# Optimization experiments

Hardware: AMD Instinct MI355X
Metric: run time of the kernel (lower is better)

## Reference

```python
import jax, jax.numpy as jnp
import numpy as np
from jax import lax

H = 1024      # hidden_size
E = 512       # embedding_size
K = 4         # max_num_children
NCLASS = 10000
EOS = NCLASS
N = 256       # number of tree nodes (complete K-ary tree, topo order)
L = 512       # number of annotation vectors


def setup_inputs() -> dict:
    key = jax.random.key(0)
    ks = jax.random.split(key, 16)
    s = 0.05
    rootH = jax.random.normal(ks[0], (1, H), jnp.float32)
    rootC = jax.random.normal(ks[1], (1, H), jnp.float32)
    annotations = jax.random.normal(ks[2], (L, H), jnp.float32)
    values = jax.random.randint(ks[3], (N,), 0, NCLASS, jnp.int32)
    idx = np.arange(N)
    parent = jnp.asarray(np.maximum(idx - 1, 0) // K, jnp.int32)
    slot = jnp.asarray(np.maximum(idx - 1, 0) % K, jnp.int32)
    # learned parameters
    emb = jax.random.normal(ks[4], (NCLASS + 1, E), jnp.float32) * s
    W_ih = jax.random.normal(ks[5], (K, 4 * H, E + H), jnp.float32) * s
    W_hh = jax.random.normal(ks[6], (K, 4 * H, H), jnp.float32) * s
    b_ih = jax.random.normal(ks[7], (K, 4 * H), jnp.float32) * s
    b_hh = jax.random.normal(ks[8], (K, 4 * H), jnp.float32) * s
    W_att = jax.random.normal(ks[9], (H, H), jnp.float32) * s
    b_att = jax.random.normal(ks[10], (H,), jnp.float32) * s
    W_pre = jax.random.normal(ks[11], (H, 2 * H), jnp.float32) * s
    b_pre = jax.random.normal(ks[12], (H,), jnp.float32) * s
    W_out = jax.random.normal(ks[13], (NCLASS + 1, H), jnp.float32) * s
    b_out = jax.random.normal(ks[14], (NCLASS + 1,), jnp.float32) * s
    return dict(rootH=rootH, rootC=rootC, annotations=annotations, values=values,
                parent=parent, slot=slot, emb=emb, W_ih=W_ih, W_hh=W_hh,
                b_ih=b_ih, b_hh=b_hh, W_att=W_att, b_att=b_att,
                W_pre=W_pre, b_pre=b_pre, W_out=W_out, b_out=b_out)


def reference(rootH, rootC, annotations, values, parent, slot, emb,
              W_ih, W_hh, b_ih, b_hh, W_att, b_att, W_pre, b_pre, W_out, b_out):
    # attention_hidden(annotations), computed once (align_type=1)
    ahv = annotations @ W_att.T + b_att            # [L, H]
    rootH0, rootC0 = rootH[0], rootC[0]            # [H]

    def step(carry, xs):
        Hbuf, Cbuf, etbuf, loss = carry
        i, v, p, k = xs
        # child LSTMCell update from parent state (slot k picks the cell)
        x = jnp.concatenate([emb[values[p]], etbuf[p]])            # [E+H]
        gates = W_ih[k] @ x + b_ih[k] + W_hh[k] @ Hbuf[p] + b_hh[k]  # [4H]
        ig, fg, gg, og = jnp.split(gates, 4)
        c_child = jax.nn.sigmoid(fg) * Cbuf[p] + jax.nn.sigmoid(ig) * jnp.tanh(gg)
        h_child = jax.nn.sigmoid(og) * jnp.tanh(c_child)
        is_root = i == 0
        h = jnp.where(is_root, rootH0, h_child)
        c = jnp.where(is_root, rootC0, c_child)
        # attention over annotations (softmax over L)
        att_logits = ahv @ h                                        # [L]
        probs = jax.nn.softmax(att_logits)
        ctx = probs @ annotations                                   # [H]
        et = jnp.tanh(W_pre @ jnp.concatenate([h, ctx]) + b_pre)    # [H]
        # output: softmax then CrossEntropyLoss (faithful double softmax)
        out_logits = W_out @ et + b_out                             # [NCLASS+1]
        p_out = jax.nn.softmax(out_logits)
        ls = jax.nn.log_softmax(p_out)
        nl = -ls[v]
        nl = jnp.where(v == EOS, nl / 5.0, nl)
        Hbuf = Hbuf.at[i].set(h)
        Cbuf = Cbuf.at[i].set(c)
        etbuf = etbuf.at[i].set(et)
        return (Hbuf, Cbuf, etbuf, loss + nl), None

    z = jnp.zeros((N, H), jnp.float32)
    init = (z, z, z, jnp.float32(0.0))
    xs = (jnp.arange(N, dtype=jnp.int32), values, parent, slot)
    (Hb, Cb, eb, loss), _ = lax.scan(step, init, xs)
    return loss
```

## Files before the change

kernel.cpp:

```cpp
#include <hip/hip_runtime.h>
#include <hip/hip_bf16.h>
#include <math.h>

#define HD 1024
#define NCLS 10001

typedef short s16x8 __attribute__((ext_vector_type(8)));
typedef unsigned short u16x8 __attribute__((ext_vector_type(8)));
typedef float f32x4 __attribute__((ext_vector_type(4)));
#define MFMA16(a_, b_, c_) __builtin_amdgcn_mfma_f32_16x16x32_bf16((a_), (b_), (c_), 0, 0, 0)

__device__ __forceinline__ float sigf(float x){ return 1.f/(1.f+__expf(-x)); }
__device__ __forceinline__ float tanhfast(float x){
  x = fminf(fmaxf(x,-10.f),10.f);
  float e2 = __expf(2.f*x);
  return (e2-1.f)/(e2+1.f);
}
__device__ __forceinline__ unsigned short f2bf(float f){
  unsigned int u = __float_as_uint(f);
  u += 0x7FFF + ((u >> 16) & 1);
  return (unsigned short)(u >> 16);
}
__device__ __forceinline__ u16x8 pack8(float4 a, float4 b){
  u16x8 r;
  r[0]=f2bf(a.x); r[1]=f2bf(a.y); r[2]=f2bf(a.z); r[3]=f2bf(a.w);
  r[4]=f2bf(b.x); r[5]=f2bf(b.y); r[6]=f2bf(b.z); r[7]=f2bf(b.w);
  return r;
}

__global__ __launch_bounds__(256) void k_cvt8(const float* __restrict__ A, unsigned short* __restrict__ B, int n){
  int i = (blockIdx.x*256 + threadIdx.x)*8;
  if (i < n){
    float4 a = *(const float4*)(A+i);
    float4 b = *(const float4*)(A+i+4);
    *(u16x8*)(B+i) = pack8(a,b);
  }
}

__global__ __launch_bounds__(256) void k_cvtw8(const float* __restrict__ Wih, const float* __restrict__ Whh,
                                               unsigned short* __restrict__ Wb){
  unsigned e8 = (blockIdx.x*256 + threadIdx.x)*8;
  unsigned sr = e8 / 2560;
  unsigned c  = e8 - sr*2560;
  const float* src = (c < 1536) ? (Wih + (size_t)sr*1536 + c) : (Whh + (size_t)sr*1024 + (c-1536));
  float4 a = *(const float4*)src;
  float4 b = *(const float4*)(src+4);
  *(u16x8*)(Wb + e8) = pack8(a,b);
}

__global__ __launch_bounds__(256) void k_cvtpre8(const float* __restrict__ Wpre,
                                                 unsigned short* __restrict__ Bpre, unsigned short* __restrict__ Wc){
  unsigned idx8 = (blockIdx.x*256 + threadIdx.x)*8;
  unsigned row = idx8 >> 11, c = idx8 & 2047;
  float4 a = *(const float4*)(Wpre + idx8);
  float4 b = *(const float4*)(Wpre + idx8 + 4);
  unsigned short* d = (c < 1024) ? (Bpre + (size_t)row*1536 + c) : (Wc + (size_t)row*1024 + (c-1024));
  *(u16x8*)d = pack8(a,b);
}

__global__ __launch_bounds__(256) void k_root(const float* __restrict__ rH, const float* __restrict__ rC,
                                              float* __restrict__ Hb, float* __restrict__ Cb,
                                              unsigned short* __restrict__ XH){
  int t = blockIdx.x*256 + threadIdx.x;
  if (t < HD){ Hb[t]=rH[t]; Cb[t]=rC[t]; XH[t]=f2bf(rH[t]); }
}

__global__ __launch_bounds__(256) void k_xasm(const float* __restrict__ emb, const int* __restrict__ values,
                                              const unsigned short* __restrict__ Etb, const unsigned short* __restrict__ XH,
                                              unsigned short* __restrict__ X, int s, int e){
  int i = s + blockIdx.x;
  if (i >= e) return;
  int slot = (i - s) & 3, j = (i - s) >> 2;
  int p = (i - 1) >> 2;
  unsigned short* xr = X + ((size_t)slot*48 + j) * 2560;
  int tid = threadIdx.x;
  const float* er = emb + (size_t)values[p] * 512;
  if (tid < 64) {
    int c = tid*8;
    float4 a = *(const float4*)(er+c);
    float4 b = *(const float4*)(er+c+4);
    *(u16x8*)(xr+c) = pack8(a,b);
  }
  const unsigned short* et = Etb + (size_t)p * 1024;
  for (int c = tid*4; c < 1024*4; c += 256*4) {}
  for (int c = tid; c < 256; c += 256) {
    ((u16x8*)(xr+512))[c]  = ((const u16x8*)et)[c];
  }
  const unsigned short* hp = XH + (size_t)p * 1536;
  for (int c = tid; c < 128; c += 256) {
    ((u16x8*)(xr+1536))[c] = ((const u16x8*)hp)[c];
  }
  if (tid >= 128 && tid < 256) {
    int c = tid - 128;
    ((u16x8*)(xr+1536))[c+0] = ((const u16x8*)hp)[c+0];
  }
}

template<int MT>
__global__ __launch_bounds__(256) void k_gemm_fb(
    const unsigned short* __restrict__ A, int astride,
    const unsigned short* __restrict__ B, int K,
    const float* __restrict__ bias,
    float* __restrict__ Cf, unsigned short* __restrict__ Cb16,
    int ostride, int coff, int N, int M)
{
  const int mb0 = blockIdx.y * (MT*16);
  const int wv = threadIdx.x >> 6, lane = threadIdx.x & 63;
  const int col = (blockIdx.x*4 + wv)*16 + (lane & 15);
  const int colc = min(col, N-1);
  const int khalf = (lane >> 4) * 8;

  f32x4 acc[MT];
  #pragma unroll
  for (int m = 0; m < MT; ++m) acc[m] = (f32x4){0.f,0.f,0.f,0.f};
  int arow[MT];
  #pragma unroll
  for (int m = 0; m < MT; ++m) arow[m] = min(mb0 + m*16 + (lane & 15), M-1);

  #pragma unroll 4
  for (int kk = 0; kk < K; kk += 32) {
    int kb = kk + khalf;
    s16x8 bfv = *(const s16x8*)(B + (size_t)colc*K + kb);
    #pragma unroll
    for (int m = 0; m < MT; ++m) {
      s16x8 af = *(const s16x8*)(A + (size_t)arow[m]*astride + kb);
      acc[m] = MFMA16(af, bfv, acc[m]);
    }
  }

  const int r0 = (lane >> 4) * 4;
  #pragma unroll
  for (int m = 0; m < MT; ++m) {
    #pragma unroll
    for (int q = 0; q < 4; ++q) {
      int row = mb0 + m*16 + r0 + q;
      if (row < M && col < N) {
        float v = acc[m][q] + (bias ? bias[col] : 0.f);
        size_t off = (size_t)row*ostride + col + coff;
        if (Cb16) Cb16[off] = f2bf(v); else Cf[off] = v;
      }
    }
  }
}

template<int MT, int KITER>
__global__ __launch_bounds__(256) void k_gemm_skzb(
    const unsigned short* __restrict__ A,
    const unsigned short* __restrict__ B, int K,
    float* __restrict__ P, int N, int Mbase, int Mpad,
    int aZ, int bZ, int KS)
{
  const int z = blockIdx.z;
  const int M = (Mbase - z + 3) >> 2;
  const unsigned short* Az = A + (size_t)z*aZ;
  const unsigned short* Bz = B + (size_t)z*bZ;
  const int ks = blockIdx.y;
  const int k0 = ks * (KITER*32);
  const int wv = threadIdx.x >> 6, lane = threadIdx.x & 63;
  const int col = (blockIdx.x*4 + wv)*16 + (lane & 15);
  const int colc = min(col, N-1);
  const int khalf = (lane >> 4) * 8;

  f32x4 acc[MT];
  #pragma unroll
  for (int m = 0; m < MT; ++m) acc[m] = (f32x4){0.f,0.f,0.f,0.f};
  int arow[MT];
  #pragma unroll
  for (int m = 0; m < MT; ++m) arow[m] = min(m*16 + (lane & 15), M-1);

  #pragma unroll 4
  for (int kk = 0; kk < KITER*32; kk += 32) {
    int kb = k0 + kk + khalf;
    s16x8 bfv = *(const s16x8*)(Bz + (size_t)colc*K + kb);
    #pragma unroll
    for (int m = 0; m < MT; ++m) {
      s16x8 af = *(const s16x8*)(Az + (size_t)arow[m]*K + kb);
      acc[m] = MFMA16(af, bfv, acc[m]);
    }
  }

  const int r0 = (lane >> 4) * 4;
  #pragma unroll
  for (int m = 0; m < MT; ++m) {
    #pragma unroll
    for (int q = 0; q < 4; ++q) {
      int row = m*16 + r0 + q;
      if (row < M && col < N)
        P[(((size_t)z*KS + ks)*Mpad + row)*N + col] = acc[m][q];
    }
  }
}

template<int MT>
__global__ __launch_bounds__(256) void k_gemm_skb(
    const unsigned short* __restrict__ A, int astride,
    const unsigned short* __restrict__ B, int K,
    float* __restrict__ P, int N, int M)
{
  const int ks = blockIdx.y;
  const int k0 = ks * 128;
  const int wv = threadIdx.x >> 6, lane = threadIdx.x & 63;
  const int col = (blockIdx.x*4 + wv)*16 + (lane & 15);
  const int colc = min(col, N-1);
  const int khalf = (lane >> 4) * 8;

  f32x4 acc[MT];
  #pragma unroll
  for (int m = 0; m < MT; ++m) acc[m] = (f32x4){0.f,0.f,0.f,0.f};
  int arow[MT];
  #pragma unroll
  for (int m = 0; m < MT; ++m) arow[m] = min(m*16 + (lane & 15), M-1);

  #pragma unroll
  for (int kk = 0; kk < 128; kk += 32) {
    int kb = k0 + kk + khalf;
    s16x8 bfv = *(const s16x8*)(B + (size_t)colc*K + kb);
    #pragma unroll
    for (int m = 0; m < MT; ++m) {
      s16x8 af = *(const s16x8*)(A + (size_t)arow[m]*astride + kb);
      acc[m] = MFMA16(af, bfv, acc[m]);
    }
  }

  const int r0 = (lane >> 4) * 4;
  #pragma unroll
  for (int m = 0; m < MT; ++m) {
    #pragma unroll
    for (int q = 0; q < 4; ++q) {
      int row = m*16 + r0 + q;
      if (row < M && col < N)
        P[((size_t)ks*M + row)*N + col] = acc[m][q];
    }
  }
}

__global__ __launch_bounds__(256) void k_red(const float* __restrict__ P, int KS, int M, int N,
                                             const float* __restrict__ bias, int tanh_flag,
                                             float* __restrict__ Cf, unsigned short* __restrict__ Cb16,
                                             int ostride)
{
  int idx = blockIdx.x*256 + threadIdx.x;
  if (idx >= M*N) return;
  int row = idx / N, col = idx - row*N;
  float s = bias ? bias[col] : 0.f;
  for (int ks = 0; ks < KS; ++ks) s += P[((size_t)ks*M + row)*N + col];
  if (tanh_flag) s = tanhfast(s);
  if (Cb16) Cb16[(size_t)row*ostride + col] = f2bf(s);
  else      Cf  [(size_t)row*ostride + col] = s;
}

__global__ __launch_bounds__(256) void k_soft(const float* __restrict__ P, int KS, int M,
                                              unsigned short* __restrict__ dst)
{
  __shared__ float sm[512];
  __shared__ float red[8];
  const int m = blockIdx.x;
  const int tid = threadIdx.x, wv = tid>>6, ln = tid&63;
  for (int l = tid; l < 512; l += 256) {
    float s = 0.f;
    for (int ks = 0; ks < KS; ++ks) s += P[((size_t)ks*M + m)*512 + l];
    sm[l] = s;
  }
  __syncthreads();
  float mx = -1e30f;
  for (int l=tid; l<512; l+=256) mx = fmaxf(mx, sm[l]);
  #pragma unroll
  for (int o=32;o;o>>=1) mx = fmaxf(mx, __shfl_xor(mx,o,64));
  if (ln==0) red[wv]=mx;
  __syncthreads();
  mx = fmaxf(fmaxf(red[0],red[1]),fmaxf(red[2],red[3]));
  float se = 0.f;
  for (int l=tid; l<512; l+=256){ float ev=__expf(sm[l]-mx); sm[l]=ev; se+=ev; }
  __syncthreads();
  #pragma unroll
  for (int o=32;o;o>>=1) se += __shfl_xor(se,o,64);
  if (ln==0) red[wv]=se;
  __syncthreads();
  float invS = 1.f/(red[0]+red[1]+red[2]+red[3]);
  for (int l=tid; l<512; l+=256) dst[(size_t)m*1536 + l] = f2bf(sm[l]*invS);
}

__global__ __launch_bounds__(256) void k_epi(const float* __restrict__ P,
                                             const float* __restrict__ b_ih, const float* __restrict__ b_hh,
                                             float* __restrict__ Hb, float* __restrict__ Cb,
                                             unsigned short* __restrict__ XH, int s, int e){
  int i = s + blockIdx.x;
  if (i >= e) return;
  int slot = (i - s) & 3, j = (i - s) >> 2;
  int p = (i - 1) >> 2;
  const float* bi = b_ih + (size_t)slot*4096;
  const float* bh = b_hh + (size_t)slot*4096;
  for (int u = threadIdx.x; u < 1024; u += 256) {
    float ig = bi[u]      + bh[u];
    float fg = bi[1024+u] + bh[1024+u];
    float gg = bi[2048+u] + bh[2048+u];
    float og = bi[3072+u] + bh[3072+u];
    #pragma unroll
    for (int ks = 0; ks < 5; ++ks) {
      const float* g = P + (((size_t)slot*5 + ks)*48 + j)*4096;
      ig += g[u]; fg += g[1024+u]; gg += g[2048+u]; og += g[3072+u];
    }
    float cp = Cb[(size_t)p*1024 + u];
    float c  = sigf(fg)*cp + sigf(ig)*tanhfast(gg);
    float h  = sigf(og)*tanhfast(c);
    Hb[(size_t)i*1024+u] = h;
    Cb[(size_t)i*1024+u] = c;
    XH[(size_t)i*1536+u] = f2bf(h);
  }
}

__global__ __launch_bounds__(256) void k_loss(const float* __restrict__ Lg,
                                              const int* __restrict__ values,
                                              float* __restrict__ Nl)
{
  __shared__ float red[8];
  const int node = blockIdx.x;
  const int tid = threadIdx.x, wv = tid>>6, ln = tid&63;
  const float* lg = Lg + (size_t)node*NCLS;

  float m = -1e30f;
  for (int i=tid;i<NCLS;i+=256) m = fmaxf(m, lg[i]);
  #pragma unroll
  for (int o=32;o;o>>=1) m = fmaxf(m, __shfl_xor(m,o,64));
  if (ln==0) red[wv]=m;
  __syncthreads();
  m = fmaxf(fmaxf(red[0],red[1]),fmaxf(red[2],red[3]));
  __syncthreads();

  float s = 0.f;
  for (int i=tid;i<NCLS;i+=256) s += __expf(lg[i]-m);
  #pragma unroll
  for (int o=32;o;o>>=1) s += __shfl_xor(s,o,64);
  if (ln==0) red[wv]=s;
  __syncthreads();
  s = red[0]+red[1]+red[2]+red[3];
  __syncthreads();
  float invs = 1.f/s;

  float q = 0.f;
  for (int i=tid;i<NCLS;i+=256) q += __expf(__expf(lg[i]-m)*invs);
  #pragma unroll
  for (int o=32;o;o>>=1) q += __shfl_xor(q,o,64);
  if (ln==0) red[wv]=q;
  __syncthreads();
  if (tid==0) {
    float qq = red[0]+red[1]+red[2]+red[3];
    int v = values[node];
    float pv = __expf(lg[v]-m)*invs;
    float nl = __logf(qq) - pv;
    if (v == NCLS-1) nl *= 0.2f;
    Nl[node] = nl;
  }
}

__global__ __launch_bounds__(256) void k_final(const float* __restrict__ Nl, float* __restrict__ out){
  __shared__ float red[8];
  int tid = threadIdx.x, wv = tid>>6, ln = tid&63;
  float s = Nl[tid];
  #pragma unroll
  for (int o=32;o;o>>=1) s += __shfl_xor(s,o,64);
  if (ln==0) red[wv]=s;
  __syncthreads();
  if (tid==0) out[0] = red[0]+red[1]+red[2]+red[3];
}

static inline void gemm_skb(hipStream_t st, int MT, const unsigned short* A, int astride,
                            const unsigned short* B, int K, float* P, int N, int M)
{
  dim3 grid(N/64, K/128);
  #define SKCASE(MTv) k_gemm_skb<MTv><<<grid, 256, 0, st>>>(A,astride,B,K,P,N,M)
  switch(MT){
    case 1:  SKCASE(1);  break;
    case 4:  SKCASE(4);  break;
    case 11: SKCASE(11); break;
    default: SKCASE(16); break;
  }
  #undef SKCASE
}

extern "C" void kernel_launch(void* const* d_in, const int* in_sizes, int n_in,
                              void* d_out, int out_size, void* d_ws, size_t ws_size,
                              hipStream_t stream)
{
  const float* rootH = (const float*)d_in[0];
  const float* rootC = (const float*)d_in[1];
  const float* ann   = (const float*)d_in[2];
  const int*   values= (const int*)d_in[3];
  const float* emb   = (const float*)d_in[6];
  const float* W_ih  = (const float*)d_in[7];
  const float* W_hh  = (const float*)d_in[8];
  const float* b_ih  = (const float*)d_in[9];
  const float* b_hh  = (const float*)d_in[10];
  const float* W_att = (const float*)d_in[11];
  const float* b_att = (const float*)d_in[12];
  const float* W_pre = (const float*)d_in[13];
  const float* b_pre = (const float*)d_in[14];
  const float* W_out = (const float*)d_in[15];
  const float* b_out = (const float*)d_in[16];

  float* ws = (float*)d_ws;
  float* Hb  = ws; ws += 256*1024;
  float* Cb  = ws; ws += 256*1024;
  float* Lg  = ws; ws += (size_t)256*NCLS;
  float* Nl  = ws; ws += 256;
  float* PB  = ws; ws += 4*5*48*4096;
  unsigned short* Wb    = (unsigned short*)ws;
  unsigned short* Woutb = Wb    + (size_t)4*4096*2560;
  unsigned short* Wattb = Woutb + (size_t)NCLS*1024;
  unsigned short* Bpre  = Wattb + 1024*1024;
  unsigned short* Wpcb  = Bpre  + 1024*1536;
  unsigned short* AHVb  = Wpcb  + 1024*1024;
  unsigned short* Annb  = AHVb  + 512*1024;
  unsigned short* XH    = Annb  + 512*1024;
  unsigned short* Etb   = XH    + 256*1536;
  unsigned short* Xb    = Etb   + 256*1024;

  k_cvt8  <<<256,   256, 0, stream>>>(ann,   Annb,  512*1024);
  k_cvt8  <<<512,   256, 0, stream>>>(W_att, Wattb, 1024*1024);
  k_cvt8  <<<5001,  256, 0, stream>>>(W_out, Woutb, NCLS*1024);
  k_cvtw8 <<<20480, 256, 0, stream>>>(W_ih, W_hh, Wb);
  k_cvtpre8<<<1024, 256, 0, stream>>>(W_pre, Bpre, Wpcb);
  k_gemm_fb<4><<<dim3(16,8),  256, 0, stream>>>(Annb, 1024, Wattb, 1024, b_att, nullptr, AHVb, 1024, 0, 1024, 512);
  k_gemm_fb<4><<<dim3(8,16),  256, 0, stream>>>(Wpcb, 1024, Annb, 1024, nullptr, nullptr, Bpre, 1536, 1024, 512, 1024);
  k_root<<<4, 256, 0, stream>>>(rootH, rootC, Hb, Cb, XH);

  const int LS[6] = {0,1,5,21,85,256};
  for (int lev=0; lev<5; ++lev){
    int s=LS[lev], e=LS[lev+1], n=e-s;
    if (lev>0){
      k_xasm<<<n,256,0,stream>>>(emb, values, Etb, XH, Xb, s, e);
      if (lev==4)
        k_gemm_skzb<3,16><<<dim3(64,5,4),256,0,stream>>>(Xb, Wb, 2560, PB, 4096, n, 48, 48*2560, 4096*2560, 5);
      else
        k_gemm_skzb<1,16><<<dim3(64,5,4),256,0,stream>>>(Xb, Wb, 2560, PB, 4096, n, 48, 48*2560, 4096*2560, 5);
      k_epi<<<n,256,0,stream>>>(PB, b_ih, b_hh, Hb, Cb, XH, s, e);
    }
    int mtn = (n+15)/16;
    gemm_skb(stream, mtn, XH + (size_t)s*1536, 1536, AHVb, 1024, PB, 512, n);
    k_soft<<<n,256,0,stream>>>(PB, 8, n, XH + (size_t)s*1536 + 1024);
    gemm_skb(stream, mtn, XH + (size_t)s*1536, 1536, Bpre, 1536, PB, 1024, n);
    k_red<<<(n*1024+255)/256, 256, 0, stream>>>(PB, 12, n, 1024, b_pre, 1, nullptr, Etb + (size_t)s*1024, 1024);
  }

  k_gemm_fb<4><<<dim3(157,4), 256, 0, stream>>>(Etb, 1024, Woutb, 1024, b_out, Lg, nullptr, NCLS, 0, NCLS, 256);
  k_loss <<<256,256,0,stream>>>(Lg, values, Nl);
  k_final<<<1,  256,0,stream>>>(Nl, (float*)d_out);
}
```

Measured before the change: 449.3 us.

## Widen conversion, epilogue and reduction kernels; store logits as bf16

Replaces the per-weight conversion kernels with a 32-element-per-thread converter and stores W_ih and W_hh as separate bf16 buffers. The gate GEMM now picks between the two B buffers per k-chunk, which removes the interleaving conversion. The LSTM epilogue, the split-K reduction and the xasm copy are vectorised to float4/u16x8 accesses. Output logits are written as bf16 instead of fp32, halving the logit write and the loss-kernel reads at some precision cost in the double softmax.

```diff
diff --git a/kernel.cpp b/kernel.cpp
--- a/kernel.cpp
+++ b/kernel.cpp
@@ -7,6 +7,7 @@
 
 typedef short s16x8 __attribute__((ext_vector_type(8)));
 typedef unsigned short u16x8 __attribute__((ext_vector_type(8)));
+typedef unsigned short u16x4 __attribute__((ext_vector_type(4)));
 typedef float f32x4 __attribute__((ext_vector_type(4)));
 #define MFMA16(a_, b_, c_) __builtin_amdgcn_mfma_f32_16x16x32_bf16((a_), (b_), (c_), 0, 0, 0)
 
@@ -21,6 +22,9 @@
   u += 0x7FFF + ((u >> 16) & 1);
   return (unsigned short)(u >> 16);
 }
+__device__ __forceinline__ float bf2f(unsigned short u){
+  return __uint_as_float(((unsigned)u) << 16);
+}
 __device__ __forceinline__ u16x8 pack8(float4 a, float4 b){
   u16x8 r;
   r[0]=f2bf(a.x); r[1]=f2bf(a.y); r[2]=f2bf(a.z); r[3]=f2bf(a.w);
@@ -28,24 +32,17 @@
   return r;
 }
 
-__global__ __launch_bounds__(256) void k_cvt8(const float* __restrict__ A, unsigned short* __restrict__ B, int n){
-  int i = (blockIdx.x*256 + threadIdx.x)*8;
-  if (i < n){
-    float4 a = *(const float4*)(A+i);
-    float4 b = *(const float4*)(A+i+4);
-    *(u16x8*)(B+i) = pack8(a,b);
-  }
-}
-
-__global__ __launch_bounds__(256) void k_cvtw8(const float* __restrict__ Wih, const float* __restrict__ Whh,
-                                               unsigned short* __restrict__ Wb){
-  unsigned e8 = (blockIdx.x*256 + threadIdx.x)*8;
-  unsigned sr = e8 / 2560;
-  unsigned c  = e8 - sr*2560;
-  const float* src = (c < 1536) ? (Wih + (size_t)sr*1536 + c) : (Whh + (size_t)sr*1024 + (c-1536));
-  float4 a = *(const float4*)src;
-  float4 b = *(const float4*)(src+4);
-  *(u16x8*)(Wb + e8) = pack8(a,b);
+__global__ __launch_bounds__(256) void k_cvt32(const float* __restrict__ A, unsigned short* __restrict__ B, int n){
+  int i = (blockIdx.x*256 + threadIdx.x)*32;
+  if (i >= n) return;
+  float4 a0 = *(const float4*)(A+i+ 0), b0 = *(const float4*)(A+i+ 4);
+  float4 a1 = *(const float4*)(A+i+ 8), b1 = *(const float4*)(A+i+12);
+  float4 a2 = *(const float4*)(A+i+16), b2 = *(const float4*)(A+i+20);
+  float4 a3 = *(const float4*)(A+i+24), b3 = *(const float4*)(A+i+28);
+  *(u16x8*)(B+i+ 0) = pack8(a0,b0);
+  *(u16x8*)(B+i+ 8) = pack8(a1,b1);
+  *(u16x8*)(B+i+16) = pack8(a2,b2);
+  *(u16x8*)(B+i+24) = pack8(a3,b3);
 }
 
 __global__ __launch_bounds__(256) void k_cvtpre8(const float* __restrict__ Wpre,
@@ -74,25 +71,21 @@
   int p = (i - 1) >> 2;
   unsigned short* xr = X + ((size_t)slot*48 + j) * 2560;
   int tid = threadIdx.x;
-  const float* er = emb + (size_t)values[p] * 512;
   if (tid < 64) {
     int c = tid*8;
+    const float* er = emb + (size_t)values[p] * 512;
     float4 a = *(const float4*)(er+c);
     float4 b = *(const float4*)(er+c+4);
     *(u16x8*)(xr+c) = pack8(a,b);
-  }
-  const unsigned short* et = Etb + (size_t)p * 1024;
-  for (int c = tid*4; c < 1024*4; c += 256*4) {}
-  for (int c = tid; c < 256; c += 256) {
-    ((u16x8*)(xr+512))[c]  = ((const u16x8*)et)[c];
-  }
-  const unsigned short* hp = XH + (size_t)p * 1536;
-  for (int c = tid; c < 128; c += 256) {
-    ((u16x8*)(xr+1536))[c] = ((const u16x8*)hp)[c];
-  }
-  if (tid >= 128 && tid < 256) {
-    int c = tid - 128;
-    ((u16x8*)(xr+1536))[c+0] = ((const u16x8*)hp)[c+0];
+  } else if (tid < 192) {
+    int c = (tid-64)*8;
+    const unsigned short* et = Etb + (size_t)p * 1024;
+    *(u16x8*)(xr+512+c) = *(const u16x8*)(et+c);
+  } else {
+    int c = (tid-192)*16;
+    const unsigned short* hp = XH + (size_t)p * 1536;
+    *(u16x8*)(xr+1536+c)   = *(const u16x8*)(hp+c);
+    *(u16x8*)(xr+1536+c+8) = *(const u16x8*)(hp+c+8);
   }
 }
 
@@ -144,16 +137,18 @@
 }
 
 template<int MT, int KITER>
-__global__ __launch_bounds__(256) void k_gemm_skzb(
-    const unsigned short* __restrict__ A,
-    const unsigned short* __restrict__ B, int K,
+__global__ __launch_bounds__(256) void k_gemm_skzb2(
+    const unsigned short* __restrict__ A, int astride,
+    const unsigned short* __restrict__ B1, int K1,
+    const unsigned short* __restrict__ B2, int K2,
     float* __restrict__ P, int N, int Mbase, int Mpad,
-    int aZ, int bZ, int KS)
+    int aZ, int b1Z, int b2Z, int KS)
 {
   const int z = blockIdx.z;
   const int M = (Mbase - z + 3) >> 2;
   const unsigned short* Az = A + (size_t)z*aZ;
-  const unsigned short* Bz = B + (size_t)z*bZ;
+  const unsigned short* B1z = B1 + (size_t)z*b1Z;
+  const unsigned short* B2z = B2 + (size_t)z*b2Z;
   const int ks = blockIdx.y;
   const int k0 = ks * (KITER*32);
   const int wv = threadIdx.x >> 6, lane = threadIdx.x & 63;
@@ -171,10 +166,12 @@
   #pragma unroll 4
   for (int kk = 0; kk < KITER*32; kk += 32) {
     int kb = k0 + kk + khalf;
-    s16x8 bfv = *(const s16x8*)(Bz + (size_t)colc*K + kb);
+    const unsigned short* bp = (kb < K1) ? (B1z + (size_t)colc*K1 + kb)
+                                         : (B2z + (size_t)colc*K2 + (kb - K1));
+    s16x8 bfv = *(const s16x8*)bp;
     #pragma unroll
     for (int m = 0; m < MT; ++m) {
-      s16x8 af = *(const s16x8*)(Az + (size_t)arow[m]*K + kb);
+      s16x8 af = *(const s16x8*)(Az + (size_t)arow[m]*astride + kb);
       acc[m] = MFMA16(af, bfv, acc[m]);
     }
   }
@@ -234,19 +231,21 @@
   }
 }
 
-__global__ __launch_bounds__(256) void k_red(const float* __restrict__ P, int KS, int M, int N,
-                                             const float* __restrict__ bias, int tanh_flag,
-                                             float* __restrict__ Cf, unsigned short* __restrict__ Cb16,
-                                             int ostride)
-{
-  int idx = blockIdx.x*256 + threadIdx.x;
-  if (idx >= M*N) return;
-  int row = idx / N, col = idx - row*N;
-  float s = bias ? bias[col] : 0.f;
-  for (int ks = 0; ks < KS; ++ks) s += P[((size_t)ks*M + row)*N + col];
-  if (tanh_flag) s = tanhfast(s);
-  if (Cb16) Cb16[(size_t)row*ostride + col] = f2bf(s);
-  else      Cf  [(size_t)row*ostride + col] = s;
+__global__ __launch_bounds__(256) void k_red4(const float* __restrict__ P, int KS, int M, int N,
+                                              const float* __restrict__ bias, int tanh_flag,
+                                              unsigned short* __restrict__ Cb16, int ostride)
+{
+  int idx4 = (blockIdx.x*256 + threadIdx.x)*4;
+  if (idx4 >= M*N) return;
+  int row = idx4 / N, col = idx4 - row*N;
+  float4 s = *(const float4*)(bias + col);
+  for (int ks = 0; ks < KS; ++ks) {
+    float4 p = *(const float4*)(P + ((size_t)ks*M + row)*N + col);
+    s.x += p.x; s.y += p.y; s.z += p.z; s.w += p.w;
+  }
+  if (tanh_flag){ s.x=tanhfast(s.x); s.y=tanhfast(s.y); s.z=tanhfast(s.z); s.w=tanhfast(s.w); }
+  u16x4 r; r[0]=f2bf(s.x); r[1]=f2bf(s.y); r[2]=f2bf(s.z); r[3]=f2bf(s.w);
+  *(u16x4*)(Cb16 + (size_t)row*ostride + col) = r;
 }
 
 __global__ __launch_bounds__(256) void k_soft(const float* __restrict__ P, int KS, int M,
@@ -290,36 +289,48 @@
   int p = (i - 1) >> 2;
   const float* bi = b_ih + (size_t)slot*4096;
   const float* bh = b_hh + (size_t)slot*4096;
-  for (int u = threadIdx.x; u < 1024; u += 256) {
-    float ig = bi[u]      + bh[u];
-    float fg = bi[1024+u] + bh[1024+u];
-    float gg = bi[2048+u] + bh[2048+u];
-    float og = bi[3072+u] + bh[3072+u];
-    #pragma unroll
-    for (int ks = 0; ks < 5; ++ks) {
-      const float* g = P + (((size_t)slot*5 + ks)*48 + j)*4096;
-      ig += g[u]; fg += g[1024+u]; gg += g[2048+u]; og += g[3072+u];
-    }
-    float cp = Cb[(size_t)p*1024 + u];
-    float c  = sigf(fg)*cp + sigf(ig)*tanhfast(gg);
-    float h  = sigf(og)*tanhfast(c);
-    Hb[(size_t)i*1024+u] = h;
-    Cb[(size_t)i*1024+u] = c;
-    XH[(size_t)i*1536+u] = f2bf(h);
-  }
-}
-
-__global__ __launch_bounds__(256) void k_loss(const float* __restrict__ Lg,
+  const int u = threadIdx.x*4;
+
+  float4 ig, fg, gg, og;
+  {
+    float4 a, b;
+    a = *(const float4*)(bi+u);      b = *(const float4*)(bh+u);      ig = make_float4(a.x+b.x,a.y+b.y,a.z+b.z,a.w+b.w);
+    a = *(const float4*)(bi+1024+u); b = *(const float4*)(bh+1024+u); fg = make_float4(a.x+b.x,a.y+b.y,a.z+b.z,a.w+b.w);
+    a = *(const float4*)(bi+2048+u); b = *(const float4*)(bh+2048+u); gg = make_float4(a.x+b.x,a.y+b.y,a.z+b.z,a.w+b.w);
+    a = *(const float4*)(bi+3072+u); b = *(const float4*)(bh+3072+u); og = make_float4(a.x+b.x,a.y+b.y,a.z+b.z,a.w+b.w);
+  }
+  #pragma unroll
+  for (int ks = 0; ks < 5; ++ks) {
+    const float* g = P + (((size_t)slot*5 + ks)*48 + j)*4096;
+    float4 a;
+    a = *(const float4*)(g+u);      ig.x+=a.x; ig.y+=a.y; ig.z+=a.z; ig.w+=a.w;
+    a = *(const float4*)(g+1024+u); fg.x+=a.x; fg.y+=a.y; fg.z+=a.z; fg.w+=a.w;
+    a = *(const float4*)(g+2048+u); gg.x+=a.x; gg.y+=a.y; gg.z+=a.z; gg.w+=a.w;
+    a = *(const float4*)(g+3072+u); og.x+=a.x; og.y+=a.y; og.z+=a.z; og.w+=a.w;
+  }
+  float4 cp = *(const float4*)(Cb + (size_t)p*1024 + u);
+  float4 cc, hh;
+  cc.x = sigf(fg.x)*cp.x + sigf(ig.x)*tanhfast(gg.x); hh.x = sigf(og.x)*tanhfast(cc.x);
+  cc.y = sigf(fg.y)*cp.y + sigf(ig.y)*tanhfast(gg.y); hh.y = sigf(og.y)*tanhfast(cc.y);
+  cc.z = sigf(fg.z)*cp.z + sigf(ig.z)*tanhfast(gg.z); hh.z = sigf(og.z)*tanhfast(cc.z);
+  cc.w = sigf(fg.w)*cp.w + sigf(ig.w)*tanhfast(gg.w); hh.w = sigf(og.w)*tanhfast(cc.w);
+  *(float4*)(Hb + (size_t)i*1024 + u) = hh;
+  *(float4*)(Cb + (size_t)i*1024 + u) = cc;
+  u16x4 r; r[0]=f2bf(hh.x); r[1]=f2bf(hh.y); r[2]=f2bf(hh.z); r[3]=f2bf(hh.w);
+  *(u16x4*)(XH + (size_t)i*1536 + u) = r;
+}
+
+__global__ __launch_bounds__(256) void k_loss(const unsigned short* __restrict__ Lgb,
                                               const int* __restrict__ values,
                                               float* __restrict__ Nl)
 {
   __shared__ float red[8];
   const int node = blockIdx.x;
   const int tid = threadIdx.x, wv = tid>>6, ln = tid&63;
-  const float* lg = Lg + (size_t)node*NCLS;
+  const unsigned short* lg = Lgb + (size_t)node*NCLS;
 
   float m = -1e30f;
-  for (int i=tid;i<NCLS;i+=256) m = fmaxf(m, lg[i]);
+  for (int i=tid;i<NCLS;i+=256) m = fmaxf(m, bf2f(lg[i]));
   #pragma unroll
   for (int o=32;o;o>>=1) m = fmaxf(m, __shfl_xor(m,o,64));
   if (ln==0) red[wv]=m;
@@ -328,7 +339,7 @@
   __syncthreads();
 
   float s = 0.f;
-  for (int i=tid;i<NCLS;i+=256) s += __expf(lg[i]-m);
+  for (int i=tid;i<NCLS;i+=256) s += __expf(bf2f(lg[i])-m);
   #pragma unroll
   for (int o=32;o;o>>=1) s += __shfl_xor(s,o,64);
   if (ln==0) red[wv]=s;
@@ -338,7 +349,7 @@
   float invs = 1.f/s;
 
   float q = 0.f;
-  for (int i=tid;i<NCLS;i+=256) q += __expf(__expf(lg[i]-m)*invs);
+  for (int i=tid;i<NCLS;i+=256) q += __expf(__expf(bf2f(lg[i])-m)*invs);
   #pragma unroll
   for (int o=32;o;o>>=1) q += __shfl_xor(q,o,64);
   if (ln==0) red[wv]=q;
@@ -346,7 +357,7 @@
   if (tid==0) {
     float qq = red[0]+red[1]+red[2]+red[3];
     int v = values[node];
-    float pv = __expf(lg[v]-m)*invs;
+    float pv = __expf(bf2f(lg[v])-m)*invs;
     float nl = __logf(qq) - pv;
     if (v == NCLS-1) nl *= 0.2f;
     Nl[node] = nl;
@@ -401,11 +412,11 @@
   float* ws = (float*)d_ws;
   float* Hb  = ws; ws += 256*1024;
   float* Cb  = ws; ws += 256*1024;
-  float* Lg  = ws; ws += (size_t)256*NCLS;
   float* Nl  = ws; ws += 256;
   float* PB  = ws; ws += 4*5*48*4096;
-  unsigned short* Wb    = (unsigned short*)ws;
-  unsigned short* Woutb = Wb    + (size_t)4*4096*2560;
+  unsigned short* Wbih  = (unsigned short*)ws;
+  unsigned short* Wbhh  = Wbih  + (size_t)4*4096*1536;
+  unsigned short* Woutb = Wbhh  + (size_t)4*4096*1024;
   unsigned short* Wattb = Woutb + (size_t)NCLS*1024;
   unsigned short* Bpre  = Wattb + 1024*1024;
   unsigned short* Wpcb  = Bpre  + 1024*1536;
@@ -414,11 +425,13 @@
   unsigned short* XH    = Annb  + 512*1024;
   unsigned short* Etb   = XH    + 256*1536;
   unsigned short* Xb    = Etb   + 256*1024;
-
-  k_cvt8  <<<256,   256, 0, stream>>>(ann,   Annb,  512*1024);
-  k_cvt8  <<<512,   256, 0, stream>>>(W_att, Wattb, 1024*1024);
-  k_cvt8  <<<5001,  256, 0, stream>>>(W_out, Woutb, NCLS*1024);
-  k_cvtw8 <<<20480, 256, 0, stream>>>(W_ih, W_hh, Wb);
+  unsigned short* Lgb   = Xb    + 4*48*2560;
+
+  k_cvt32 <<<3072, 256, 0, stream>>>(W_ih,  Wbih,  4*4096*1536);
+  k_cvt32 <<<2048, 256, 0, stream>>>(W_hh,  Wbhh,  4*4096*1024);
+  k_cvt32 <<<1251, 256, 0, stream>>>(W_out, Woutb, NCLS*1024);
+  k_cvt32 <<<64,   256, 0, stream>>>(ann,   Annb,  512*1024);
+  k_cvt32 <<<128,  256, 0, stream>>>(W_att, Wattb, 1024*1024);
   k_cvtpre8<<<1024, 256, 0, stream>>>(W_pre, Bpre, Wpcb);
   k_gemm_fb<4><<<dim3(16,8),  256, 0, stream>>>(Annb, 1024, Wattb, 1024, b_att, nullptr, AHVb, 1024, 0, 1024, 512);
   k_gemm_fb<4><<<dim3(8,16),  256, 0, stream>>>(Wpcb, 1024, Annb, 1024, nullptr, nullptr, Bpre, 1536, 1024, 512, 1024);
@@ -430,19 +443,21 @@
     if (lev>0){
       k_xasm<<<n,256,0,stream>>>(emb, values, Etb, XH, Xb, s, e);
       if (lev==4)
-        k_gemm_skzb<3,16><<<dim3(64,5,4),256,0,stream>>>(Xb, Wb, 2560, PB, 4096, n, 48, 48*2560, 4096*2560, 5);
+        k_gemm_skzb2<3,16><<<dim3(64,5,4),256,0,stream>>>(Xb, 2560, Wbih, 1536, Wbhh, 1024, PB,
+            4096, n, 48, 48*2560, 4096*1536, 4096*1024, 5);
       else
-        k_gemm_skzb<1,16><<<dim3(64,5,4),256,0,stream>>>(Xb, Wb, 2560, PB, 4096, n, 48, 48*2560, 4096*2560, 5);
+        k_gemm_skzb2<1,16><<<dim3(64,5,4),256,0,stream>>>(Xb, 2560, Wbih, 1536, Wbhh, 1024, PB,
+            4096, n, 48, 48*2560, 4096*1536, 4096*1024, 5);
       k_epi<<<n,256,0,stream>>>(PB, b_ih, b_hh, Hb, Cb, XH, s, e);
     }
     int mtn = (n+15)/16;
     gemm_skb(stream, mtn, XH + (size_t)s*1536, 1536, AHVb, 1024, PB, 512, n);
     k_soft<<<n,256,0,stream>>>(PB, 8, n, XH + (size_t)s*1536 + 1024);
     gemm_skb(stream, mtn, XH + (size_t)s*1536, 1536, Bpre, 1536, PB, 1024, n);
-    k_red<<<(n*1024+255)/256, 256, 0, stream>>>(PB, 12, n, 1024, b_pre, 1, nullptr, Etb + (size_t)s*1024, 1024);
-  }
-
-  k_gemm_fb<4><<<dim3(157,4), 256, 0, stream>>>(Etb, 1024, Woutb, 1024, b_out, Lg, nullptr, NCLS, 0, NCLS, 256);
-  k_loss <<<256,256,0,stream>>>(Lg, values, Nl);
+    k_red4<<<(n*1024/4+255)/256, 256, 0, stream>>>(PB, 12, n, 1024, b_pre, 1, Etb + (size_t)s*1024, 1024);
+  }
+
+  k_gemm_fb<4><<<dim3(157,4), 256, 0, stream>>>(Etb, 1024, Woutb, 1024, b_out, nullptr, Lgb, NCLS, 0, NCLS, 256);
+  k_loss <<<256,256,0,stream>>>(Lgb, values, Nl);
   k_final<<<1,  256,0,stream>>>(Nl, (float*)d_out);
 }
```

Measured after the change: 458.4 us. +2.0%, slower.
